# Kernel tuning notes

Measured on AMD Instinct MI355X. Metric: run time of the kernel, lower is better.

The kernel has to match this reference:

```python
import jax, jax.numpy as jnp
import numpy as np

BT = 64  # chunk size

def _l2norm(x, eps=1e-6):
    n = jnp.linalg.norm(x, axis=-1, keepdims=True)
    return x / jnp.maximum(n, eps)

def _kda_gate(g_raw, A_log, dt_bias):
    # g = -exp(A_log) * softplus(g_raw + dt_bias); broadcast A_log over K
    return -jnp.exp(A_log)[None, None, :, None] * jax.nn.softplus(g_raw.astype(jnp.float32) + dt_bias[None, None].astype(jnp.float32))

def _chunk_kda_fwd(q, k, v, g, beta):
    B, T, H, K = q.shape
    V = v.shape[-1]
    assert T % BT == 0
    NT = T // BT
    scale = K ** -0.5
    q = _l2norm(q.astype(jnp.float32)) * scale
    k = _l2norm(k.astype(jnp.float32))

    def to_chunks(x, d):
        # [B,T,H,d] -> [NT,B,H,BT,d]
        return x.astype(jnp.float32).transpose(0, 2, 1, 3).reshape(B, H, NT, BT, d).transpose(2, 0, 1, 3, 4)

    qc, kc, vc, gc = to_chunks(q, K), to_chunks(k, K), to_chunks(v, V), to_chunks(g, K)
    bc = beta.astype(jnp.float32).transpose(0, 2, 1).reshape(B, H, NT, BT).transpose(2, 0, 1, 3)  # [NT,B,H,BT]

    eye = jnp.eye(BT, dtype=jnp.float32)
    tril_strict = jnp.tril(jnp.ones((BT, BT), bool), -1)
    tril_incl = jnp.tril(jnp.ones((BT, BT), bool), 0)

    def body(S, xs):
        q_i, k_i, v_i, g_i, b_i = xs  # [B,H,BT,*]
        gcum = jnp.cumsum(g_i, axis=-2)                              # [B,H,BT,K]
        diff = gcum[:, :, :, None, :] - gcum[:, :, None, :, :]      # [B,H,BT,BT,K]
        decay = jnp.exp(jnp.minimum(diff, 0.0))
        # intra-chunk k-k matrix, beta row-scaled, strictly lower, negated
        Akk = jnp.einsum('bhik,bhjk,bhijk->bhij', k_i, k_i, decay)
        M = -jnp.where(tril_strict, Akk * b_i[..., :, None], 0.0)
        # UT transform: torch in-place loop solves Tm = (I - M)^{-1}
        Tm = jax.scipy.linalg.solve_triangular(eye - M, jnp.broadcast_to(eye, M.shape), lower=True)
        Afin = Tm * b_i[..., None, :]                                # column scale by beta
        k_eg = k_i * jnp.exp(gcum)
        w = Afin @ k_eg                                              # [B,H,BT,K]
        u = Afin @ v_i                                               # [B,H,BT,V]
        Aqk = jnp.einsum('bhik,bhjk,bhijk->bhij', q_i, k_i, decay)
        Aqk = jnp.where(tril_incl, Aqk, 0.0)
        v_new = u - w @ S
        o_i = (q_i * jnp.exp(gcum)) @ S + Aqk @ v_new
        g_last = gcum[:, :, -1, :]                                   # [B,H,K]
        k_dec = jnp.exp(g_last[:, :, None, :] - gcum) * k_i
        S_new = S * jnp.exp(g_last)[..., None] + jnp.einsum('bhck,bhcv->bhkv', k_dec, v_new)
        return S_new, o_i

    S0 = jnp.zeros((B, H, K, V), jnp.float32)
    _, o = jax.lax.scan(body, S0, (qc, kc, vc, gc, bc))              # o: [NT,B,H,BT,V]
    return o.transpose(1, 2, 0, 3, 4).reshape(B, H, T, V).transpose(0, 2, 1, 3)


def setup_inputs() -> dict:
    key = jax.random.key(0)
    ks = jax.random.split(key, 7)
    B, T, H, K, V = 2, 8192, 16, 32, 64
    return {
        'q': jax.random.normal(ks[0], (B, T, H, K), jnp.float32),
        'k': jax.random.normal(ks[1], (B, T, H, K), jnp.float32),
        'v': jax.random.normal(ks[2], (B, T, H, V), jnp.float32),
        'g_raw': jax.random.normal(ks[3], (B, T, H, K), jnp.float32),
        'beta': jax.random.uniform(ks[4], (B, T, H), jnp.float32),
        'A_log': jax.random.normal(ks[5], (H,), jnp.float32) - 3.0,  # moderate decay rate
        'dt_bias': jax.random.normal(ks[6], (H, K), jnp.float32) * 0.1,
    }


def reference(q, k, v, g_raw, beta, A_log, dt_bias):
    g = _kda_gate(g_raw, A_log, dt_bias)
    return _chunk_kda_fwd(q, k, v, g, beta)
```

## Files before the change

kernel.cpp:

```cpp
#include <hip/hip_runtime.h>
#include <math.h>

#define Tt 8192
#define Hh 16
#define NCH 4096

#define OFF_U   ((size_t)NCH*2048)
#define OFF_M   ((size_t)NCH*6144)
#define OFF_C   ((size_t)NCH*7168)
#define OFF_MS  ((size_t)NCH*9216)
#define OFF_CS  (OFF_MS + (size_t)256*1024)
#define OFF_SS  (OFF_CS + (size_t)256*2048)

__device__ __forceinline__ float softplusf(float x) {
  return fmaxf(x, 0.f) + log1pf(__expf(-fabsf(x)));
}

__global__ __launch_bounds__(256) void kda_phase1(
    const float* __restrict__ kin, const float* __restrict__ vin,
    const float* __restrict__ graw, const float* __restrict__ beta,
    const float* __restrict__ A_log, const float* __restrict__ dt_bias,
    float* __restrict__ ws)
{
  __shared__ float sG[64*33];
  __shared__ float sK[64*33];
  __shared__ float sL[64*64];
  __shared__ float sT[64*65];
  __shared__ float sC2[3*272];
  __shared__ float sEgl[32];

  const int tid = threadIdx.x;
  const int ch = blockIdx.x;
  const int c = ch >> 5, bh = ch & 31;
  const int b = bh >> 4, h = bh & 15;
  const int t0 = c*64;
  const int iq = tid >> 2, kq = (tid & 3)*8;

  float* wsW = ws;
  float* wsU = ws + OFF_U;
  float* wsM = ws + OFF_M;
  float* wsCc= ws + OFF_C;

  const float negA = -__expf(A_log[h]);

  {
    const float* gr = graw + (((size_t)b*Tt + t0 + iq)*Hh + h)*32 + kq;
    const float* db = dt_bias + h*32 + kq;
    #pragma unroll
    for (int r = 0; r < 8; ++r)
      sG[iq*33 + kq + r] = negA * softplusf(gr[r] + db[r]);
  }
  __syncthreads();
  if (tid < 32) {
    float acc = 0.f;
    for (int i = 0; i < 64; ++i) { acc += sG[i*33 + tid]; sG[i*33 + tid] = acc; }
  }
  {
    const float* kp = kin + (((size_t)b*Tt + t0 + iq)*Hh + h)*32 + kq;
    float kr[8]; float ss = 0.f;
    #pragma unroll
    for (int r = 0; r < 8; ++r) { kr[r] = kp[r]; ss += kr[r]*kr[r]; }
    ss += __shfl_xor(ss, 1); ss += __shfl_xor(ss, 2);
    const float sc = 1.f / fmaxf(sqrtf(ss), 1e-6f);
    #pragma unroll
    for (int r = 0; r < 8; ++r) sK[iq*33 + kq + r] = kr[r]*sc;
  }
  __syncthreads();

  const float b_cm = beta[((size_t)b*Tt + t0 + (tid & 63))*Hh + h];
  float* P  = sT;
  float* Qb = sT + 2112;
  const int i64 = tid & 63, jj2 = (tid >> 6)*2;
  for (int jt = 0; jt < 8; ++jt) {
    const int j0 = jt*8;
    #pragma unroll
    for (int r = 0; r < 8; ++r) {
      const int idx = iq*33 + kq + r;
      P[idx] = sK[idx] * __expf(fminf(sG[idx] - sG[j0*33 + kq + r], 0.f));
    }
    {
      const int jj = tid >> 5, kk = tid & 31;
      Qb[jj*32 + kk] = sK[(j0+jj)*33 + kk] * __expf(sG[j0*33 + kk] - sG[(j0+jj)*33 + kk]);
    }
    __syncthreads();
    float a0 = 0.f, a1 = 0.f;
    #pragma unroll
    for (int hf = 0; hf < 2; ++hf) {
      const int k0 = hf*16;
      float qa[16], qb[16];
      #pragma unroll
      for (int t4 = 0; t4 < 4; ++t4) {
        float4 xa = *(const float4*)(Qb + (jj2  )*32 + k0 + t4*4);
        float4 xb = *(const float4*)(Qb + (jj2+1)*32 + k0 + t4*4);
        qa[t4*4+0]=xa.x; qa[t4*4+1]=xa.y; qa[t4*4+2]=xa.z; qa[t4*4+3]=xa.w;
        qb[t4*4+0]=xb.x; qb[t4*4+1]=xb.y; qb[t4*4+2]=xb.z; qb[t4*4+3]=xb.w;
      }
      #pragma unroll
      for (int kk = 0; kk < 16; ++kk) {
        const float p = P[i64*33 + k0 + kk];
        a0 += p * qa[kk]; a1 += p * qb[kk];
      }
    }
    const int j_0 = j0 + jj2;
    sL[(j_0  )*64 + i64] = (i64 > j_0  ) ? a0*b_cm : 0.f;
    sL[(j_0+1)*64 + i64] = (i64 > j_0+1) ? a1*b_cm : 0.f;
    __syncthreads();
  }

  for (int e = tid; e < 4096; e += 256) {
    const int row = e >> 6, col = e & 63;
    sT[row*65 + col] = (row == col) ? 1.f : 0.f;
  }
  __syncthreads();
  if (tid < 64) {
    const int p = tid >> 4, col = tid & 15;
    for (int i = 1; i < 16; ++i) {
      const int gi = p*16 + i, gc = p*16 + col;
      float acc = 0.f;
      for (int j = 0; j < i; ++j)
        acc -= sL[(p*16+j)*64 + gi] * sT[(p*16+j)*65 + gc];
      sT[gi*65 + gc] = acc + ((i == col) ? 1.f : 0.f);
    }
  }
  __syncthreads();
  {
    const int wid = tid >> 6;
    const int lane = tid & 63;
    const int ri = lane & 15, c4 = (lane >> 4)*4;
    auto offblk = [&](int p, int q) {
      float a0=0.f, a1=0.f, a2=0.f, a3=0.f;
      for (int m = q; m < p; ++m) {
        #pragma unroll
        for (int j = 0; j < 16; ++j) {
          const float lv = sL[(m*16+j)*64 + p*16+ri];
          const float* tp = sT + (m*16+j)*65 + q*16 + c4;
          a0 += lv*tp[0]; a1 += lv*tp[1]; a2 += lv*tp[2]; a3 += lv*tp[3];
        }
      }
      float* cp = sC2 + wid*272 + ri*17 + c4;
      cp[0]=a0; cp[1]=a1; cp[2]=a2; cp[3]=a3;
      float b0=0.f, b1=0.f, b2=0.f, b3=0.f;
      #pragma unroll
      for (int j = 0; j < 16; ++j) {
        const float tv = sT[(p*16+ri)*65 + p*16 + j];
        const float* cj = sC2 + wid*272 + j*17 + c4;
        b0 += tv*cj[0]; b1 += tv*cj[1]; b2 += tv*cj[2]; b3 += tv*cj[3];
      }
      float* op = sT + (p*16+ri)*65 + q*16 + c4;
      op[0]=-b0; op[1]=-b1; op[2]=-b2; op[3]=-b3;
    };
    if (wid == 0) offblk(1,0); else if (wid == 1) offblk(2,1); else if (wid == 2) offblk(3,2);
    __syncthreads();
    if (wid == 0) offblk(2,0); else if (wid == 1) offblk(3,1);
    __syncthreads();
    if (wid == 0) offblk(3,0);
  }
  __syncthreads();

  {
    const float b_row = beta[((size_t)b*Tt + t0 + iq)*Hh + h];
    #pragma unroll
    for (int r = 0; r < 8; ++r) {
      const int idx = iq*33 + kq + r;
      const float g = sG[idx], kn = sK[idx];
      sL[iq*32 + kq + r] = b_row * kn * __expf(g);
      sK[idx] = kn * __expf(sG[63*33 + kq + r] - g);
    }
    if (tid < 32) sEgl[tid] = __expf(sG[63*33 + tid]);
  }
  __syncthreads();

  {
    float acc[8] = {0,0,0,0,0,0,0,0};
    for (int j = 0; j <= iq; ++j) {
      const float t = sT[iq*65 + j];
      const float4 e0 = *(const float4*)(sL + j*32 + kq);
      const float4 e1 = *(const float4*)(sL + j*32 + kq + 4);
      acc[0]+=t*e0.x; acc[1]+=t*e0.y; acc[2]+=t*e0.z; acc[3]+=t*e0.w;
      acc[4]+=t*e1.x; acc[5]+=t*e1.y; acc[6]+=t*e1.z; acc[7]+=t*e1.w;
    }
    #pragma unroll
    for (int r = 0; r < 8; ++r) {
      wsW[(size_t)ch*2048 + tid*8 + r] = acc[r];
      sG[iq*32 + kq + r] = acc[r];
    }
  }
  __syncthreads();

  {
    #pragma unroll
    for (int r = 0; r < 4; ++r) {
      const int f = tid + 256*r;
      const int j = f >> 4, qd = f & 15;
      const float bj = beta[((size_t)b*Tt + t0 + j)*Hh + h];
      float4 v4 = *(const float4*)(vin + (((size_t)b*Tt + t0 + j)*Hh + h)*64 + qd*4);
      v4.x *= bj; v4.y *= bj; v4.z *= bj; v4.w *= bj;
      *(float4*)(sL + j*64 + qd*4) = v4;
    }
  }
  __syncthreads();

  float uacc[16];
  {
    const int vs = (tid & 3)*16;
    #pragma unroll
    for (int r = 0; r < 16; ++r) uacc[r] = 0.f;
    for (int j = 0; j <= iq; ++j) {
      const float t = sT[iq*65 + j];
      const float4 e0 = *(const float4*)(sL + j*64 + vs);
      const float4 e1 = *(const float4*)(sL + j*64 + vs + 4);
      const float4 e2 = *(const float4*)(sL + j*64 + vs + 8);
      const float4 e3 = *(const float4*)(sL + j*64 + vs + 12);
      uacc[0]+=t*e0.x;  uacc[1]+=t*e0.y;  uacc[2]+=t*e0.z;  uacc[3]+=t*e0.w;
      uacc[4]+=t*e1.x;  uacc[5]+=t*e1.y;  uacc[6]+=t*e1.z;  uacc[7]+=t*e1.w;
      uacc[8]+=t*e2.x;  uacc[9]+=t*e2.y;  uacc[10]+=t*e2.z; uacc[11]+=t*e2.w;
      uacc[12]+=t*e3.x; uacc[13]+=t*e3.y; uacc[14]+=t*e3.z; uacc[15]+=t*e3.w;
    }
    #pragma unroll
    for (int rr = 0; rr < 4; ++rr) {
      float4 o4; o4.x=uacc[rr*4]; o4.y=uacc[rr*4+1]; o4.z=uacc[rr*4+2]; o4.w=uacc[rr*4+3];
      *(float4*)(wsU + (size_t)ch*4096 + tid*16 + rr*4) = o4;
    }
  }
  __syncthreads();
  {
    const int vs = (tid & 3)*16;
    #pragma unroll
    for (int rr = 0; rr < 4; ++rr) {
      float4 o4; o4.x=uacc[rr*4]; o4.y=uacc[rr*4+1]; o4.z=uacc[rr*4+2]; o4.w=uacc[rr*4+3];
      *(float4*)(sL + iq*64 + vs + rr*4) = o4;
    }
  }
  __syncthreads();

  {
    const int a = tid >> 3, b4 = (tid & 7)*4, v8 = (tid & 7)*8;
    float mA[4] = {0,0,0,0};
    float cA[8] = {0,0,0,0,0,0,0,0};
    for (int t = 0; t < 64; ++t) {
      const float kd = sK[t*33 + a];
      const float4 wv = *(const float4*)(sG + t*32 + b4);
      mA[0]+=kd*wv.x; mA[1]+=kd*wv.y; mA[2]+=kd*wv.z; mA[3]+=kd*wv.w;
      const float4 u0 = *(const float4*)(sL + t*64 + v8);
      const float4 u1 = *(const float4*)(sL + t*64 + v8 + 4);
      cA[0]+=kd*u0.x; cA[1]+=kd*u0.y; cA[2]+=kd*u0.z; cA[3]+=kd*u0.w;
      cA[4]+=kd*u1.x; cA[5]+=kd*u1.y; cA[6]+=kd*u1.z; cA[7]+=kd*u1.w;
    }
    float4 m4;
    m4.x = ((a == b4+0) ? sEgl[a] : 0.f) - mA[0];
    m4.y = ((a == b4+1) ? sEgl[a] : 0.f) - mA[1];
    m4.z = ((a == b4+2) ? sEgl[a] : 0.f) - mA[2];
    m4.w = ((a == b4+3) ? sEgl[a] : 0.f) - mA[3];
    *(float4*)(wsM + (size_t)ch*1024 + tid*4) = m4;
    float4 c0, c1;
    c0.x=cA[0]; c0.y=cA[1]; c0.z=cA[2]; c0.w=cA[3];
    c1.x=cA[4]; c1.y=cA[5]; c1.z=cA[6]; c1.w=cA[7];
    *(float4*)(wsCc + (size_t)ch*2048 + tid*8) = c0;
    *(float4*)(wsCc + (size_t)ch*2048 + tid*8 + 4) = c1;
  }
}

__global__ __launch_bounds__(256) void kda_scanA(float* __restrict__ ws)
{
  __shared__ float sMa[32*33];
  __shared__ float sMc[32*33];
  __shared__ float sCa[32*18];
  const int tid = threadIdx.x;
  const int vt = blockIdx.x & 3, seg = (blockIdx.x >> 2) & 7, bh = blockIdx.x >> 5;
  const int v0 = vt*16;
  const int a = tid >> 3, b4 = (tid & 7)*4, c2 = (tid & 7)*2;
  const float* wsM = ws + OFF_M;
  const float* wsC = ws + OFF_C;

  #pragma unroll
  for (int r = 0; r < 4; ++r) sMa[a*33 + b4 + r] = (a == b4 + r) ? 1.f : 0.f;
  sCa[a*18 + c2] = 0.f; sCa[a*18 + c2 + 1] = 0.f;
  __syncthreads();

  for (int i = 0; i < 16; ++i) {
    const int ch = (seg*16 + i)*32 + bh;
    float4 m4 = *(const float4*)(wsM + (size_t)ch*1024 + tid*4);
    float2 cc = *(const float2*)(wsC + (size_t)ch*2048 + a*64 + v0 + c2);
    sMc[a*33+b4+0]=m4.x; sMc[a*33+b4+1]=m4.y; sMc[a*33+b4+2]=m4.z; sMc[a*33+b4+3]=m4.w;
    __syncthreads();
    float cn0 = cc.x, cn1 = cc.y;
    float mn0=0.f, mn1=0.f, mn2=0.f, mn3=0.f;
    for (int bb = 0; bb < 32; ++bb) {
      const float m = sMc[a*33 + bb];
      const float2 s2 = *(const float2*)(sCa + bb*18 + c2);
      cn0 += m*s2.x; cn1 += m*s2.y;
      mn0 += m*sMa[bb*33+b4+0]; mn1 += m*sMa[bb*33+b4+1];
      mn2 += m*sMa[bb*33+b4+2]; mn3 += m*sMa[bb*33+b4+3];
    }
    __syncthreads();
    sCa[a*18+c2] = cn0; sCa[a*18+c2+1] = cn1;
    sMa[a*33+b4+0]=mn0; sMa[a*33+b4+1]=mn1; sMa[a*33+b4+2]=mn2; sMa[a*33+b4+3]=mn3;
    __syncthreads();
  }
  const size_t sid = (size_t)(bh*8 + seg);
  float* wsMs = ws + OFF_MS;
  float* wsCs = ws + OFF_CS;
  if (vt == 0) {
    #pragma unroll
    for (int r = 0; r < 4; ++r) wsMs[sid*1024 + tid*4 + r] = sMa[a*33+b4+r];
  }
  float2 co; co.x = sCa[a*18+c2]; co.y = sCa[a*18+c2+1];
  *(float2*)(wsCs + sid*2048 + a*64 + v0 + c2) = co;
}

__global__ __launch_bounds__(256) void kda_scanB(float* __restrict__ ws)
{
  __shared__ float sS[32*64];
  __shared__ float sM[32*33];
  __shared__ float sC2[32*64];
  const int tid = threadIdx.x;
  const int bh = blockIdx.x;
  const int a = tid >> 3, b4 = (tid & 7)*4, v8 = (tid & 7)*8;
  const float* wsMs = ws + OFF_MS;
  const float* wsCs = ws + OFF_CS;
  float* wsSs = ws + OFF_SS;

  #pragma unroll
  for (int r = 0; r < 8; ++r) sS[a*64 + v8 + r] = 0.f;
  __syncthreads();
  for (int seg = 0; seg < 8; ++seg) {
    const size_t sid = (size_t)(bh*8 + seg);
    #pragma unroll
    for (int r = 0; r < 8; ++r) wsSs[sid*2048 + tid*8 + r] = sS[a*64+v8+r];
    float4 m4 = *(const float4*)(wsMs + sid*1024 + tid*4);
    float4 c0 = *(const float4*)(wsCs + sid*2048 + tid*8);
    float4 c1 = *(const float4*)(wsCs + sid*2048 + tid*8 + 4);
    sM[a*33+b4+0]=m4.x; sM[a*33+b4+1]=m4.y; sM[a*33+b4+2]=m4.z; sM[a*33+b4+3]=m4.w;
    sC2[a*64+v8+0]=c0.x; sC2[a*64+v8+1]=c0.y; sC2[a*64+v8+2]=c0.z; sC2[a*64+v8+3]=c0.w;
    sC2[a*64+v8+4]=c1.x; sC2[a*64+v8+5]=c1.y; sC2[a*64+v8+6]=c1.z; sC2[a*64+v8+7]=c1.w;
    __syncthreads();
    float n0=0,n1=0,n2=0,n3=0,n4=0,n5=0,n6=0,n7=0;
    for (int bb = 0; bb < 32; ++bb) {
      const float m = sM[a*33 + bb];
      const float4 s0 = *(const float4*)(sS + bb*64 + v8);
      const float4 s1 = *(const float4*)(sS + bb*64 + v8 + 4);
      n0 += m*s0.x; n1 += m*s0.y; n2 += m*s0.z; n3 += m*s0.w;
      n4 += m*s1.x; n5 += m*s1.y; n6 += m*s1.z; n7 += m*s1.w;
    }
    n0 += sC2[a*64+v8+0]; n1 += sC2[a*64+v8+1]; n2 += sC2[a*64+v8+2]; n3 += sC2[a*64+v8+3];
    n4 += sC2[a*64+v8+4]; n5 += sC2[a*64+v8+5]; n6 += sC2[a*64+v8+6]; n7 += sC2[a*64+v8+7];
    __syncthreads();
    sS[a*64+v8+0]=n0; sS[a*64+v8+1]=n1; sS[a*64+v8+2]=n2; sS[a*64+v8+3]=n3;
    sS[a*64+v8+4]=n4; sS[a*64+v8+5]=n5; sS[a*64+v8+6]=n6; sS[a*64+v8+7]=n7;
    __syncthreads();
  }
}

__global__ __launch_bounds__(256) void kda_scanC(float* __restrict__ ws)
{
  __shared__ float sM[32*33];
  __shared__ float sS[32*18];
  const int tid = threadIdx.x;
  const int vt = blockIdx.x & 3, seg = (blockIdx.x >> 2) & 7, bh = blockIdx.x >> 5;
  const int v0 = vt*16;
  const int a = tid >> 3, b4 = (tid & 7)*4, c2 = (tid & 7)*2;
  const float* wsM = ws + OFF_M;
  float* wsC = ws + OFF_C;
  const float* wsSs = ws + OFF_SS;

  const size_t sid = (size_t)(bh*8 + seg);
  {
    float2 s0 = *(const float2*)(wsSs + sid*2048 + a*64 + v0 + c2);
    sS[a*18 + c2] = s0.x; sS[a*18 + c2 + 1] = s0.y;
  }
  __syncthreads();

  for (int i = 0; i < 16; ++i) {
    const int ch = (seg*16 + i)*32 + bh;
    float4 m4 = *(const float4*)(wsM + (size_t)ch*1024 + tid*4);
    float2 cc = *(const float2*)(wsC + (size_t)ch*2048 + a*64 + v0 + c2);
    sM[a*33+b4+0]=m4.x; sM[a*33+b4+1]=m4.y; sM[a*33+b4+2]=m4.z; sM[a*33+b4+3]=m4.w;
    float2 se; se.x = sS[a*18+c2]; se.y = sS[a*18+c2+1];
    *(float2*)(wsC + (size_t)ch*2048 + a*64 + v0 + c2) = se;
    __syncthreads();
    float n0 = cc.x, n1 = cc.y;
    for (int bb = 0; bb < 32; ++bb) {
      const float m = sM[a*33 + bb];
      const float2 s2 = *(const float2*)(sS + bb*18 + c2);
      n0 += m*s2.x; n1 += m*s2.y;
    }
    __syncthreads();
    sS[a*18+c2] = n0; sS[a*18+c2+1] = n1;
    __syncthreads();
  }
}

__global__ __launch_bounds__(256) void kda_phase3(
    const float* __restrict__ qin, const float* __restrict__ kin,
    const float* __restrict__ graw,
    const float* __restrict__ A_log, const float* __restrict__ dt_bias,
    const float* __restrict__ ws, float* __restrict__ out)
{
  __shared__ float sG[64*33];
  __shared__ float sQ[64*33];
  __shared__ float sA[64*65];
  __shared__ float sV[64*64];

  const int tid = threadIdx.x;
  const int ch = blockIdx.x;
  const int c = ch >> 5, bh = ch & 31;
  const int b = bh >> 4, h = bh & 15;
  const int t0 = c*64;
  const int iq = tid >> 2, kq = (tid & 3)*8;

  const float* wsW = ws;
  const float* wsU = ws + OFF_U;
  const float* wsS = ws + OFF_C;

  const float negA = -__expf(A_log[h]);
  {
    const float* gr = graw + (((size_t)b*Tt + t0 + iq)*Hh + h)*32 + kq;
    const float* db = dt_bias + h*32 + kq;
    #pragma unroll
    for (int r = 0; r < 8; ++r)
      sG[iq*33 + kq + r] = negA * softplusf(gr[r] + db[r]);
  }
  __syncthreads();
  if (tid < 32) {
    float acc = 0.f;
    for (int i = 0; i < 64; ++i) { acc += sG[i*33 + tid]; sG[i*33 + tid] = acc; }
  }
  float knr[8];
  {
    const float* qp = qin + (((size_t)b*Tt + t0 + iq)*Hh + h)*32 + kq;
    float qr[8]; float ssq = 0.f;
    #pragma unroll
    for (int r = 0; r < 8; ++r) { qr[r] = qp[r]; ssq += qr[r]*qr[r]; }
    ssq += __shfl_xor(ssq, 1); ssq += __shfl_xor(ssq, 2);
    const float scq = 0.17677669529663687f / fmaxf(sqrtf(ssq), 1e-6f);
    #pragma unroll
    for (int r = 0; r < 8; ++r) sQ[iq*33 + kq + r] = qr[r]*scq;

    const float* kp = kin + (((size_t)b*Tt + t0 + iq)*Hh + h)*32 + kq;
    float ssk = 0.f;
    #pragma unroll
    for (int r = 0; r < 8; ++r) { knr[r] = kp[r]; ssk += knr[r]*knr[r]; }
    ssk += __shfl_xor(ssk, 1); ssk += __shfl_xor(ssk, 2);
    const float sck = 1.f / fmaxf(sqrtf(ssk), 1e-6f);
    #pragma unroll
    for (int r = 0; r < 8; ++r) knr[r] *= sck;
  }
  __syncthreads();

  float* P  = sV;
  float* Qb = sV + 2112;
  const int i64 = tid & 63, jj2 = (tid >> 6)*2;
  for (int jt = 0; jt < 8; ++jt) {
    const int j0 = jt*8;
    #pragma unroll
    for (int r = 0; r < 8; ++r) {
      const int idx = iq*33 + kq + r;
      P[idx] = sQ[idx] * __expf(fminf(sG[idx] - sG[j0*33 + kq + r], 0.f));
    }
    if (iq >= j0 && iq < j0 + 8) {
      const int jj = iq - j0;
      #pragma unroll
      for (int r = 0; r < 8; ++r)
        Qb[jj*32 + kq + r] = knr[r] * __expf(sG[j0*33 + kq + r] - sG[iq*33 + kq + r]);
    }
    __syncthreads();
    float a0 = 0.f, a1 = 0.f;
    #pragma unroll
    for (int hf = 0; hf < 2; ++hf) {
      const int k0 = hf*16;
      float qa[16], qb[16];
      #pragma unroll
      for (int t4 = 0; t4 < 4; ++t4) {
        float4 xa = *(const float4*)(Qb + (jj2  )*32 + k0 + t4*4);
        float4 xb = *(const float4*)(Qb + (jj2+1)*32 + k0 + t4*4);
        qa[t4*4+0]=xa.x; qa[t4*4+1]=xa.y; qa[t4*4+2]=xa.z; qa[t4*4+3]=xa.w;
        qb[t4*4+0]=xb.x; qb[t4*4+1]=xb.y; qb[t4*4+2]=xb.z; qb[t4*4+3]=xb.w;
      }
      #pragma unroll
      for (int kk = 0; kk < 16; ++kk) {
        const float p = P[i64*33 + k0 + kk];
        a0 += p * qa[kk]; a1 += p * qb[kk];
      }
    }
    const int j_0 = j0 + jj2;
    sA[i64*65 + j_0  ] = (i64 >= j_0  ) ? a0 : 0.f;
    sA[i64*65 + j_0+1] = (i64 >= j_0+1) ? a1 : 0.f;
    __syncthreads();
  }

  float qgr[8];
  {
    #pragma unroll
    for (int r = 0; r < 8; ++r) {
      const int idx = iq*33 + kq + r;
      qgr[r] = sQ[idx] * __expf(sG[idx]);
    }
  }
  __syncthreads();
  {
    #pragma unroll
    for (int rr = 0; rr < 2; ++rr) {
      const int f = tid + 256*rr;
      *(float4*)(sG + f*4) = *(const float4*)(wsS + (size_t)ch*2048 + f*4);
    }
    *(float4*)(sV + tid*8)     = *(const float4*)(wsW + (size_t)ch*2048 + tid*8);
    *(float4*)(sV + tid*8 + 4) = *(const float4*)(wsW + (size_t)ch*2048 + tid*8 + 4);
  }
  __syncthreads();
  {
    float qe[8];
    #pragma unroll
    for (int r = 0; r < 8; ++r) qe[r] = qgr[r];
    for (int j = 0; j <= iq; ++j) {
      const float av = sA[iq*65 + j];
      const float4 w0 = *(const float4*)(sV + j*32 + kq);
      const float4 w1 = *(const float4*)(sV + j*32 + kq + 4);
      qe[0]-=av*w0.x; qe[1]-=av*w0.y; qe[2]-=av*w0.z; qe[3]-=av*w0.w;
      qe[4]-=av*w1.x; qe[5]-=av*w1.y; qe[6]-=av*w1.z; qe[7]-=av*w1.w;
    }
    #pragma unroll
    for (int r = 0; r < 8; ++r) sQ[iq*33 + kq + r] = qe[r];
  }
  __syncthreads();
  {
    #pragma unroll
    for (int rr = 0; rr < 4; ++rr) {
      const int f = tid + 256*rr;
      *(float4*)(sV + f*4) = *(const float4*)(wsU + (size_t)ch*4096 + f*4);
    }
  }
  __syncthreads();
  {
    const int vs = (tid & 3)*16;
    float acc[16];
    #pragma unroll
    for (int r = 0; r < 16; ++r) acc[r] = 0.f;
    for (int kk = 0; kk < 32; ++kk) {
      const float qv = sQ[iq*33 + kk];
      const float4 s0 = *(const float4*)(sG + kk*64 + vs);
      const float4 s1 = *(const float4*)(sG + kk*64 + vs + 4);
      const float4 s2 = *(const float4*)(sG + kk*64 + vs + 8);
      const float4 s3 = *(const float4*)(sG + kk*64 + vs + 12);
      acc[0]+=qv*s0.x;  acc[1]+=qv*s0.y;  acc[2]+=qv*s0.z;  acc[3]+=qv*s0.w;
      acc[4]+=qv*s1.x;  acc[5]+=qv*s1.y;  acc[6]+=qv*s1.z;  acc[7]+=qv*s1.w;
      acc[8]+=qv*s2.x;  acc[9]+=qv*s2.y;  acc[10]+=qv*s2.z; acc[11]+=qv*s2.w;
      acc[12]+=qv*s3.x; acc[13]+=qv*s3.y; acc[14]+=qv*s3.z; acc[15]+=qv*s3.w;
    }
    for (int j = 0; j <= iq; ++j) {
      const float av = sA[iq*65 + j];
      const float4 u0 = *(const float4*)(sV + j*64 + vs);
      const float4 u1 = *(const float4*)(sV + j*64 + vs + 4);
      const float4 u2 = *(const float4*)(sV + j*64 + vs + 8);
      const float4 u3 = *(const float4*)(sV + j*64 + vs + 12);
      acc[0]+=av*u0.x;  acc[1]+=av*u0.y;  acc[2]+=av*u0.z;  acc[3]+=av*u0.w;
      acc[4]+=av*u1.x;  acc[5]+=av*u1.y;  acc[6]+=av*u1.z;  acc[7]+=av*u1.w;
      acc[8]+=av*u2.x;  acc[9]+=av*u2.y;  acc[10]+=av*u2.z; acc[11]+=av*u2.w;
      acc[12]+=av*u3.x; acc[13]+=av*u3.y; acc[14]+=av*u3.z; acc[15]+=av*u3.w;
    }
    float* op = out + (((size_t)b*Tt + t0 + iq)*Hh + h)*64 + vs;
    #pragma unroll
    for (int rr = 0; rr < 4; ++rr) {
      float4 o4; o4.x=acc[rr*4]; o4.y=acc[rr*4+1]; o4.z=acc[rr*4+2]; o4.w=acc[rr*4+3];
      *(float4*)(op + rr*4) = o4;
    }
  }
}

extern "C" void kernel_launch(void* const* d_in, const int* in_sizes, int n_in,
                              void* d_out, int out_size, void* d_ws, size_t ws_size,
                              hipStream_t stream) {
  const float* q    = (const float*)d_in[0];
  const float* k    = (const float*)d_in[1];
  const float* v    = (const float*)d_in[2];
  const float* graw = (const float*)d_in[3];
  const float* beta = (const float*)d_in[4];
  const float* A_log= (const float*)d_in[5];
  const float* dtb  = (const float*)d_in[6];
  float* out = (float*)d_out;
  float* ws  = (float*)d_ws;

  kda_phase1<<<NCH, 256, 0, stream>>>(k, v, graw, beta, A_log, dtb, ws);
  kda_scanA<<<1024, 256, 0, stream>>>(ws);
  kda_scanB<<<32, 256, 0, stream>>>(ws);
  kda_scanC<<<1024, 256, 0, stream>>>(ws);
  kda_phase3<<<NCH, 256, 0, stream>>>(q, k, graw, A_log, dtb, ws, out);
}
```

Measured before the change: 572.6 us.

## Prefetch scan inputs, split scanB over V tiles, vectorize intra-chunk dot products

The three scan kernels now prefetch the next chunk's transition matrix and carry terms into registers while the current step computes, which removes one barrier per iteration. scanB is split across four V tiles (128 blocks instead of 32) to add parallelism on the serial segment scan. In phase1 and phase3 the decay-weighted P tile is padded to a 36-float row stride so it can be written and read with float4, and the cumulative-sum loop over g is blocked into register batches. The extra prefetched values raise register pressure, and the padded P tile moves Qb to a new shared-memory offset.

```diff
diff --git a/kernel.cpp b/kernel.cpp
--- a/kernel.cpp
+++ b/kernel.cpp
@@ -52,8 +52,14 @@
   }
   __syncthreads();
   if (tid < 32) {
-    float acc = 0.f;
-    for (int i = 0; i < 64; ++i) { acc += sG[i*33 + tid]; sG[i*33 + tid] = acc; }
+    float c0 = 0.f;
+    for (int blk = 0; blk < 4; ++blk) {
+      float v[16];
+      #pragma unroll
+      for (int i = 0; i < 16; ++i) v[i] = sG[(blk*16+i)*33 + tid];
+      #pragma unroll
+      for (int i = 0; i < 16; ++i) { c0 += v[i]; sG[(blk*16+i)*33 + tid] = c0; }
+    }
   }
   {
     const float* kp = kin + (((size_t)b*Tt + t0 + iq)*Hh + h)*32 + kq;
@@ -69,14 +75,19 @@
 
   const float b_cm = beta[((size_t)b*Tt + t0 + (tid & 63))*Hh + h];
   float* P  = sT;
-  float* Qb = sT + 2112;
+  float* Qb = sT + 2304;
   const int i64 = tid & 63, jj2 = (tid >> 6)*2;
   for (int jt = 0; jt < 8; ++jt) {
     const int j0 = jt*8;
-    #pragma unroll
-    for (int r = 0; r < 8; ++r) {
-      const int idx = iq*33 + kq + r;
-      P[idx] = sK[idx] * __expf(fminf(sG[idx] - sG[j0*33 + kq + r], 0.f));
+    {
+      float pv[8];
+      #pragma unroll
+      for (int r = 0; r < 8; ++r) {
+        const int idx = iq*33 + kq + r;
+        pv[r] = sK[idx] * __expf(fminf(sG[idx] - sG[j0*33 + kq + r], 0.f));
+      }
+      *(float4*)(P + iq*36 + kq)     = make_float4(pv[0],pv[1],pv[2],pv[3]);
+      *(float4*)(P + iq*36 + kq + 4) = make_float4(pv[4],pv[5],pv[6],pv[7]);
     }
     {
       const int jj = tid >> 5, kk = tid & 31;
@@ -87,18 +98,13 @@
     #pragma unroll
     for (int hf = 0; hf < 2; ++hf) {
       const int k0 = hf*16;
-      float qa[16], qb[16];
       #pragma unroll
       for (int t4 = 0; t4 < 4; ++t4) {
-        float4 xa = *(const float4*)(Qb + (jj2  )*32 + k0 + t4*4);
-        float4 xb = *(const float4*)(Qb + (jj2+1)*32 + k0 + t4*4);
-        qa[t4*4+0]=xa.x; qa[t4*4+1]=xa.y; qa[t4*4+2]=xa.z; qa[t4*4+3]=xa.w;
-        qb[t4*4+0]=xb.x; qb[t4*4+1]=xb.y; qb[t4*4+2]=xb.z; qb[t4*4+3]=xb.w;
-      }
-      #pragma unroll
-      for (int kk = 0; kk < 16; ++kk) {
-        const float p = P[i64*33 + k0 + kk];
-        a0 += p * qa[kk]; a1 += p * qb[kk];
+        const float4 pa = *(const float4*)(P  + i64*36 + k0 + t4*4);
+        const float4 xa = *(const float4*)(Qb + (jj2  )*32 + k0 + t4*4);
+        const float4 xb = *(const float4*)(Qb + (jj2+1)*32 + k0 + t4*4);
+        a0 += pa.x*xa.x + pa.y*xa.y + pa.z*xa.z + pa.w*xa.w;
+        a1 += pa.x*xb.x + pa.y*xb.y + pa.z*xb.z + pa.w*xb.w;
       }
     }
     const int j_0 = j0 + jj2;
@@ -275,14 +281,20 @@
   #pragma unroll
   for (int r = 0; r < 4; ++r) sMa[a*33 + b4 + r] = (a == b4 + r) ? 1.f : 0.f;
   sCa[a*18 + c2] = 0.f; sCa[a*18 + c2 + 1] = 0.f;
-  __syncthreads();
+
+  int ch = (seg*16)*32 + bh;
+  float4 m4 = *(const float4*)(wsM + (size_t)ch*1024 + tid*4);
+  float2 cc = *(const float2*)(wsC + (size_t)ch*2048 + a*64 + v0 + c2);
 
   for (int i = 0; i < 16; ++i) {
-    const int ch = (seg*16 + i)*32 + bh;
-    float4 m4 = *(const float4*)(wsM + (size_t)ch*1024 + tid*4);
-    float2 cc = *(const float2*)(wsC + (size_t)ch*2048 + a*64 + v0 + c2);
     sMc[a*33+b4+0]=m4.x; sMc[a*33+b4+1]=m4.y; sMc[a*33+b4+2]=m4.z; sMc[a*33+b4+3]=m4.w;
     __syncthreads();
+    float4 m4n = m4; float2 ccn = cc;
+    if (i < 15) {
+      const int chn = (seg*16 + i + 1)*32 + bh;
+      m4n = *(const float4*)(wsM + (size_t)chn*1024 + tid*4);
+      ccn = *(const float2*)(wsC + (size_t)chn*2048 + a*64 + v0 + c2);
+    }
     float cn0 = cc.x, cn1 = cc.y;
     float mn0=0.f, mn1=0.f, mn2=0.f, mn3=0.f;
     for (int bb = 0; bb < 32; ++bb) {
@@ -295,7 +307,7 @@
     __syncthreads();
     sCa[a*18+c2] = cn0; sCa[a*18+c2+1] = cn1;
     sMa[a*33+b4+0]=mn0; sMa[a*33+b4+1]=mn1; sMa[a*33+b4+2]=mn2; sMa[a*33+b4+3]=mn3;
-    __syncthreads();
+    m4 = m4n; cc = ccn;
   }
   const size_t sid = (size_t)(bh*8 + seg);
   float* wsMs = ws + OFF_MS;
@@ -310,44 +322,42 @@
 
 __global__ __launch_bounds__(256) void kda_scanB(float* __restrict__ ws)
 {
-  __shared__ float sS[32*64];
+  __shared__ float sS[32*18];
   __shared__ float sM[32*33];
-  __shared__ float sC2[32*64];
   const int tid = threadIdx.x;
-  const int bh = blockIdx.x;
-  const int a = tid >> 3, b4 = (tid & 7)*4, v8 = (tid & 7)*8;
+  const int vt = blockIdx.x & 3, bh = blockIdx.x >> 2;
+  const int v0 = vt*16;
+  const int a = tid >> 3, b4 = (tid & 7)*4, c2 = (tid & 7)*2;
   const float* wsMs = ws + OFF_MS;
   const float* wsCs = ws + OFF_CS;
   float* wsSs = ws + OFF_SS;
 
-  #pragma unroll
-  for (int r = 0; r < 8; ++r) sS[a*64 + v8 + r] = 0.f;
-  __syncthreads();
+  float s0 = 0.f, s1 = 0.f;
+  sS[a*18 + c2] = 0.f; sS[a*18 + c2 + 1] = 0.f;
+  const size_t sid0 = (size_t)(bh*8);
+  float4 m4 = *(const float4*)(wsMs + sid0*1024 + tid*4);
+  float2 cc = *(const float2*)(wsCs + sid0*2048 + a*64 + v0 + c2);
+
   for (int seg = 0; seg < 8; ++seg) {
     const size_t sid = (size_t)(bh*8 + seg);
-    #pragma unroll
-    for (int r = 0; r < 8; ++r) wsSs[sid*2048 + tid*8 + r] = sS[a*64+v8+r];
-    float4 m4 = *(const float4*)(wsMs + sid*1024 + tid*4);
-    float4 c0 = *(const float4*)(wsCs + sid*2048 + tid*8);
-    float4 c1 = *(const float4*)(wsCs + sid*2048 + tid*8 + 4);
+    *(float2*)(wsSs + sid*2048 + a*64 + v0 + c2) = make_float2(s0, s1);
     sM[a*33+b4+0]=m4.x; sM[a*33+b4+1]=m4.y; sM[a*33+b4+2]=m4.z; sM[a*33+b4+3]=m4.w;
-    sC2[a*64+v8+0]=c0.x; sC2[a*64+v8+1]=c0.y; sC2[a*64+v8+2]=c0.z; sC2[a*64+v8+3]=c0.w;
-    sC2[a*64+v8+4]=c1.x; sC2[a*64+v8+5]=c1.y; sC2[a*64+v8+6]=c1.z; sC2[a*64+v8+7]=c1.w;
-    __syncthreads();
-    float n0=0,n1=0,n2=0,n3=0,n4=0,n5=0,n6=0,n7=0;
+    __syncthreads();
+    float4 m4n = m4; float2 ccn = cc;
+    if (seg < 7) {
+      m4n = *(const float4*)(wsMs + (sid+1)*1024 + tid*4);
+      ccn = *(const float2*)(wsCs + (sid+1)*2048 + a*64 + v0 + c2);
+    }
+    float n0 = cc.x, n1 = cc.y;
     for (int bb = 0; bb < 32; ++bb) {
       const float m = sM[a*33 + bb];
-      const float4 s0 = *(const float4*)(sS + bb*64 + v8);
-      const float4 s1 = *(const float4*)(sS + bb*64 + v8 + 4);
-      n0 += m*s0.x; n1 += m*s0.y; n2 += m*s0.z; n3 += m*s0.w;
-      n4 += m*s1.x; n5 += m*s1.y; n6 += m*s1.z; n7 += m*s1.w;
-    }
-    n0 += sC2[a*64+v8+0]; n1 += sC2[a*64+v8+1]; n2 += sC2[a*64+v8+2]; n3 += sC2[a*64+v8+3];
-    n4 += sC2[a*64+v8+4]; n5 += sC2[a*64+v8+5]; n6 += sC2[a*64+v8+6]; n7 += sC2[a*64+v8+7];
-    __syncthreads();
-    sS[a*64+v8+0]=n0; sS[a*64+v8+1]=n1; sS[a*64+v8+2]=n2; sS[a*64+v8+3]=n3;
-    sS[a*64+v8+4]=n4; sS[a*64+v8+5]=n5; sS[a*64+v8+6]=n6; sS[a*64+v8+7]=n7;
-    __syncthreads();
+      const float2 s2 = *(const float2*)(sS + bb*18 + c2);
+      n0 += m*s2.x; n1 += m*s2.y;
+    }
+    __syncthreads();
+    s0 = n0; s1 = n1;
+    sS[a*18+c2] = s0; sS[a*18+c2+1] = s1;
+    m4 = m4n; cc = ccn;
   }
 }
 
@@ -364,20 +374,27 @@
   const float* wsSs = ws + OFF_SS;
 
   const size_t sid = (size_t)(bh*8 + seg);
-  {
-    float2 s0 = *(const float2*)(wsSs + sid*2048 + a*64 + v0 + c2);
-    sS[a*18 + c2] = s0.x; sS[a*18 + c2 + 1] = s0.y;
-  }
-  __syncthreads();
+  float s0, s1;
+  {
+    float2 sv = *(const float2*)(wsSs + sid*2048 + a*64 + v0 + c2);
+    s0 = sv.x; s1 = sv.y;
+    sS[a*18 + c2] = s0; sS[a*18 + c2 + 1] = s1;
+  }
+  int ch = (seg*16)*32 + bh;
+  float4 m4 = *(const float4*)(wsM + (size_t)ch*1024 + tid*4);
+  float2 cc = *(const float2*)(wsC + (size_t)ch*2048 + a*64 + v0 + c2);
 
   for (int i = 0; i < 16; ++i) {
-    const int ch = (seg*16 + i)*32 + bh;
-    float4 m4 = *(const float4*)(wsM + (size_t)ch*1024 + tid*4);
-    float2 cc = *(const float2*)(wsC + (size_t)ch*2048 + a*64 + v0 + c2);
+    const int chc = (seg*16 + i)*32 + bh;
     sM[a*33+b4+0]=m4.x; sM[a*33+b4+1]=m4.y; sM[a*33+b4+2]=m4.z; sM[a*33+b4+3]=m4.w;
-    float2 se; se.x = sS[a*18+c2]; se.y = sS[a*18+c2+1];
-    *(float2*)(wsC + (size_t)ch*2048 + a*64 + v0 + c2) = se;
-    __syncthreads();
+    *(float2*)(wsC + (size_t)chc*2048 + a*64 + v0 + c2) = make_float2(s0, s1);
+    __syncthreads();
+    float4 m4n = m4; float2 ccn = cc;
+    if (i < 15) {
+      const int chn = (seg*16 + i + 1)*32 + bh;
+      m4n = *(const float4*)(wsM + (size_t)chn*1024 + tid*4);
+      ccn = *(const float2*)(wsC + (size_t)chn*2048 + a*64 + v0 + c2);
+    }
     float n0 = cc.x, n1 = cc.y;
     for (int bb = 0; bb < 32; ++bb) {
       const float m = sM[a*33 + bb];
@@ -385,8 +402,9 @@
       n0 += m*s2.x; n1 += m*s2.y;
     }
     __syncthreads();
-    sS[a*18+c2] = n0; sS[a*18+c2+1] = n1;
-    __syncthreads();
+    s0 = n0; s1 = n1;
+    sS[a*18+c2] = s0; sS[a*18+c2+1] = s1;
+    m4 = m4n; cc = ccn;
   }
 }
 
@@ -422,8 +440,14 @@
   }
   __syncthreads();
   if (tid < 32) {
-    float acc = 0.f;
-    for (int i = 0; i < 64; ++i) { acc += sG[i*33 + tid]; sG[i*33 + tid] = acc; }
+    float c0 = 0.f;
+    for (int blk = 0; blk < 4; ++blk) {
+      float v[16];
+      #pragma unroll
+      for (int i = 0; i < 16; ++i) v[i] = sG[(blk*16+i)*33 + tid];
+      #pragma unroll
+      for (int i = 0; i < 16; ++i) { c0 += v[i]; sG[(blk*16+i)*33 + tid] = c0; }
+    }
   }
   float knr[8];
   {
@@ -448,14 +472,19 @@
   __syncthreads();
 
   float* P  = sV;
-  float* Qb = sV + 2112;
+  float* Qb = sV + 2304;
   const int i64 = tid & 63, jj2 = (tid >> 6)*2;
   for (int jt = 0; jt < 8; ++jt) {
     const int j0 = jt*8;
-    #pragma unroll
-    for (int r = 0; r < 8; ++r) {
-      const int idx = iq*33 + kq + r;
-      P[idx] = sQ[idx] * __expf(fminf(sG[idx] - sG[j0*33 + kq + r], 0.f));
+    {
+      float pv[8];
+      #pragma unroll
+      for (int r = 0; r < 8; ++r) {
+        const int idx = iq*33 + kq + r;
+        pv[r] = sQ[idx] * __expf(fminf(sG[idx] - sG[j0*33 + kq + r], 0.f));
+      }
+      *(float4*)(P + iq*36 + kq)     = make_float4(pv[0],pv[1],pv[2],pv[3]);
+      *(float4*)(P + iq*36 + kq + 4) = make_float4(pv[4],pv[5],pv[6],pv[7]);
     }
     if (iq >= j0 && iq < j0 + 8) {
       const int jj = iq - j0;
@@ -468,18 +497,13 @@
     #pragma unroll
     for (int hf = 0; hf < 2; ++hf) {
       const int k0 = hf*16;
-      float qa[16], qb[16];
       #pragma unroll
       for (int t4 = 0; t4 < 4; ++t4) {
-        float4 xa = *(const float4*)(Qb + (jj2  )*32 + k0 + t4*4);
-        float4 xb = *(const float4*)(Qb + (jj2+1)*32 + k0 + t4*4);
-        qa[t4*4+0]=xa.x; qa[t4*4+1]=xa.y; qa[t4*4+2]=xa.z; qa[t4*4+3]=xa.w;
-        qb[t4*4+0]=xb.x; qb[t4*4+1]=xb.y; qb[t4*4+2]=xb.z; qb[t4*4+3]=xb.w;
-      }
-      #pragma unroll
-      for (int kk = 0; kk < 16; ++kk) {
-        const float p = P[i64*33 + k0 + kk];
-        a0 += p * qa[kk]; a1 += p * qb[kk];
+        const float4 pa = *(const float4*)(P  + i64*36 + k0 + t4*4);
+        const float4 xa = *(const float4*)(Qb + (jj2  )*32 + k0 + t4*4);
+        const float4 xb = *(const float4*)(Qb + (jj2+1)*32 + k0 + t4*4);
+        a0 += pa.x*xa.x + pa.y*xa.y + pa.z*xa.z + pa.w*xa.w;
+        a1 += pa.x*xb.x + pa.y*xb.y + pa.z*xb.z + pa.w*xb.w;
       }
     }
     const int j_0 = j0 + jj2;
@@ -581,7 +605,7 @@
 
   kda_phase1<<<NCH, 256, 0, stream>>>(k, v, graw, beta, A_log, dtb, ws);
   kda_scanA<<<1024, 256, 0, stream>>>(ws);
-  kda_scanB<<<32, 256, 0, stream>>>(ws);
+  kda_scanB<<<128, 256, 0, stream>>>(ws);
   kda_scanC<<<1024, 256, 0, stream>>>(ws);
   kda_phase3<<<NCH, 256, 0, stream>>>(q, k, graw, A_log, dtb, ws, out);
 }
```

After: 557.1 us. -2.7%, faster.
